# Performance work log

Hardware: AMD Instinct MI355X
Metric: run time of the kernel (lower is better)

Reference implementation:

```python
import jax, jax.numpy as jnp
import numpy as np

N = 8192        # number of nodes
D_FEAT = 64     # feature dim
K = 16          # k_samples
DEG = 32        # max neighbors per node (adj built with <= DEG ones per row)
NEG = -1e30     # mask value for duplicate candidates


def setup_inputs() -> dict:
    key = jax.random.key(0)
    k1, k2, k3 = jax.random.split(key, 3)
    x = jax.random.normal(k1, (N, D_FEAT), dtype=jnp.float32)
    # adjacency with up to DEG random neighbors per row (collisions just lower degree)
    nbr = jax.random.randint(k2, (N, DEG), 0, N)
    adj = jnp.zeros((N, N), jnp.float32).at[jnp.arange(N)[:, None], nbr].set(1.0)
    current_samples = jax.random.randint(k3, (N, K), 0, N).astype(jnp.int32)
    return {"x": x, "adj": adj, "current_samples": current_samples}


def reference(x, adj, current_samples):
    n = x.shape[0]
    # padded neighbor extraction: rows of adj have at most DEG ones, so top_k of the
    # row recovers all neighbor indices; empty slots (value 0) are remapped to the
    # node itself, whose own samples are already in the candidate pool, so the
    # unique candidate set matches the torch adjacency-list construction exactly.
    vals, nbr = jax.lax.top_k(adj, DEG)                       # [N, DEG]
    self_idx = jnp.broadcast_to(jnp.arange(n, dtype=nbr.dtype)[:, None], nbr.shape)
    nbr = jnp.where(vals > 0, nbr, self_idx)
    # candidate pool: neighbor samples flattened + own samples  -> [N, C]
    cand = jnp.concatenate([current_samples[nbr].reshape(n, -1), current_samples], axis=1)
    # emulate torch.unique (sorted, dedup): sort and mask non-first occurrences
    cand = jnp.sort(cand, axis=1)                             # [N, C]
    is_first = jnp.concatenate(
        [jnp.ones((n, 1), bool), cand[:, 1:] != cand[:, :-1]], axis=1)
    # similarities x[i] . x[cand] via one gemm + gather (avoids [N, C, d] gather)
    sim_all = x @ x.T                                         # [N, N]
    sim = jnp.take_along_axis(sim_all, cand, axis=1)          # [N, C]
    sim = jnp.where(is_first, sim, NEG)                       # duplicates masked out
    top_sim, top_idx = jax.lax.top_k(sim, K)                  # [N, K]
    selected = jnp.take_along_axis(cand, top_idx, axis=1)     # [N, K]
    # rare branch: fewer than K unique candidates -> sorted uniques + pad with own samples
    nu = is_first.sum(axis=1, keepdims=True)                  # [N, 1] unique counts
    pos = jnp.cumsum(is_first, axis=1) - 1
    pos = jnp.where(is_first, pos, K)                         # dup / overflow -> dropped
    uniq_k = jnp.zeros((n, K), cand.dtype).at[
        jnp.arange(n)[:, None], pos].set(cand, mode='drop')
    j = jnp.arange(K)[None, :]
    pad = jnp.take_along_axis(current_samples, jnp.clip(j - nu, 0, K - 1), axis=1)
    out = jnp.where(nu >= K, selected, jnp.where(j < nu, uniq_k, pad))
    return out
```

## Files before the change

kernel.cpp:

```cpp
#include <hip/hip_runtime.h>
#include <math.h>

#define NN   8192
#define DF   64
#define KK   16
#define MAXNBR 33
#define NT   256
#define NBINS 2048
#define MAXC 544
#define NR   9
#define HIDX(b) ((((b) & 7) << 8) | ((b) >> 3))

typedef unsigned uvec4 __attribute__((ext_vector_type(4)));

__device__ __forceinline__ unsigned long long kmax(unsigned long long a, unsigned long long b) {
    return a > b ? a : b;
}
__device__ __forceinline__ unsigned long long kmin(unsigned long long a, unsigned long long b) {
    return a > b ? b : a;
}

__device__ __forceinline__ float row_reduce16(float acc) {
    acc += __uint_as_float(__builtin_amdgcn_update_dpp(
        0, (int)__float_as_uint(acc), 0x128, 0xF, 0xF, true));
    acc += __uint_as_float(__builtin_amdgcn_update_dpp(
        0, (int)__float_as_uint(acc), 0x124, 0xF, 0xF, true));
    acc += __uint_as_float(__builtin_amdgcn_update_dpp(
        0, (int)__float_as_uint(acc), 0x122, 0xF, 0xF, true));
    acc += __uint_as_float(__builtin_amdgcn_update_dpp(
        0, (int)__float_as_uint(acc), 0x121, 0xF, 0xF, true));
    return acc;
}

__device__ __forceinline__ void sort64_desc(unsigned long long& kv, int lane) {
    #pragma unroll
    for (int k = 2; k <= 64; k <<= 1) {
        #pragma unroll
        for (int j = k >> 1; j > 0; j >>= 1) {
            unsigned long long o = __shfl_xor(kv, j);
            bool tmax = (((lane & j) == 0) != ((lane & k) != 0));
            kv = tmax ? kmax(kv, o) : kmin(kv, o);
        }
    }
}

__global__ __launch_bounds__(NT, 8)
void fused_kernel(const float* __restrict__ x,
                  const uvec4* __restrict__ adj4,
                  const int*   __restrict__ cs,
                  int*         __restrict__ out)
{
    const int i    = blockIdx.x;
    const int t    = threadIdx.x;
    const int w    = t >> 6;
    const int lane = t & 63;

    __shared__ unsigned mask[NN / 32];
    __shared__ int nbrs[MAXNBR];
    __shared__ int nnbr;
    __shared__ alignas(16) int cand[MAXC];
    __shared__ int ncand;
    __shared__ unsigned long long histsurv[NBINS / 2];
    __shared__ unsigned sum256[NT];
    __shared__ int nsurv;
    __shared__ int B_sh;
    unsigned* const hist = reinterpret_cast<unsigned*>(histsurv);
    unsigned long long* const surv = histsurv;

    if (t < NN / 32) mask[t] = 0u;
    #pragma unroll
    for (int r = 0; r < 4; ++r) histsurv[t + NT * r] = 0ULL;
    cand[t] = 0; cand[t + NT] = 0;
    if (t < MAXC - 2 * NT) cand[t + 2 * NT] = 0;
    if (t == 0) { nbrs[0] = i; nnbr = 1; ncand = 0; nsurv = 0; }
    __syncthreads();

    const uvec4* __restrict__ row4 = adj4 + (size_t)i * (NN / 4);
    uvec4 v[8];
    #pragma unroll
    for (int u = 0; u < 8; ++u) v[u] = __builtin_nontemporal_load(&row4[t + NT * u]);
    #pragma unroll
    for (int u = 0; u < 8; ++u) {
        if ((v[u].x | v[u].y | v[u].z | v[u].w) != 0u) {
            const int base = 4 * (t + NT * u);
            const unsigned e[4] = {v[u].x, v[u].y, v[u].z, v[u].w};
            #pragma unroll
            for (int c2 = 0; c2 < 4; ++c2) {
                if (e[c2] != 0u) {
                    int s = atomicAdd(&nnbr, 1);
                    if (s < MAXNBR) nbrs[s] = base + c2;
                }
            }
        }
    }
    __syncthreads();

    const int M = min(nnbr, MAXNBR);
    const int total = M * KK;

    #pragma unroll
    for (int r = 0; r < 2; ++r) {
        int q = t + NT * r;
        if (q < total) {
            int vv = cs[(size_t)nbrs[q >> 4] * KK + (q & 15)];
            unsigned bit = 1u << (vv & 31);
            unsigned old = atomicOr(&mask[vv >> 5], bit);
            if (!(old & bit)) { int s = atomicAdd(&ncand, 1); cand[s] = vv; }
        }
    }
    const int q2 = 2 * NT + (t - 64);
    if (t >= 64 && t < 80 && q2 < total) {
        int vv = cs[(size_t)nbrs[q2 >> 4] * KK + (q2 & 15)];
        unsigned bit = 1u << (vv & 31);
        unsigned old = atomicOr(&mask[vv >> 5], bit);
        if (!(old & bit)) { int s = atomicAdd(&ncand, 1); cand[s] = vv; }
    }
    __syncthreads();

    const int ncv = ncand;

    const int g  = t >> 4;
    const int gl = t & 15;
    const float4 xi4 = reinterpret_cast<const float4*>(x + (size_t)i * DF)[gl];
    unsigned long long rkeys[NR];
    #pragma unroll
    for (int r = 0; r < NR; ++r) {
        unsigned long long key = 0ULL;
        const int c0 = 4 * g + 64 * r;
        if (c0 < ncv) {
            const int4 c4 = *reinterpret_cast<const int4*>(&cand[c0]);
            const float4 xv0 = reinterpret_cast<const float4*>(x + (size_t)c4.x * DF)[gl];
            const float4 xv1 = reinterpret_cast<const float4*>(x + (size_t)c4.y * DF)[gl];
            const float4 xv2 = reinterpret_cast<const float4*>(x + (size_t)c4.z * DF)[gl];
            const float4 xv3 = reinterpret_cast<const float4*>(x + (size_t)c4.w * DF)[gl];
            float a0 = 0.f, a1 = 0.f, a2 = 0.f, a3 = 0.f;
            a0 = fmaf(xi4.x, xv0.x, a0); a0 = fmaf(xi4.y, xv0.y, a0);
            a0 = fmaf(xi4.z, xv0.z, a0); a0 = fmaf(xi4.w, xv0.w, a0);
            a1 = fmaf(xi4.x, xv1.x, a1); a1 = fmaf(xi4.y, xv1.y, a1);
            a1 = fmaf(xi4.z, xv1.z, a1); a1 = fmaf(xi4.w, xv1.w, a1);
            a2 = fmaf(xi4.x, xv2.x, a2); a2 = fmaf(xi4.y, xv2.y, a2);
            a2 = fmaf(xi4.z, xv2.z, a2); a2 = fmaf(xi4.w, xv2.w, a2);
            a3 = fmaf(xi4.x, xv3.x, a3); a3 = fmaf(xi4.y, xv3.y, a3);
            a3 = fmaf(xi4.z, xv3.z, a3); a3 = fmaf(xi4.w, xv3.w, a3);
            a0 = row_reduce16(a0);
            a1 = row_reduce16(a1);
            a2 = row_reduce16(a2);
            a3 = row_reduce16(a3);
            if (gl < 4 && c0 + gl < ncv) {
                float av = (gl == 0) ? a0 : (gl == 1) ? a1 : (gl == 2) ? a2 : a3;
                int  vb = (gl == 0) ? c4.x : (gl == 1) ? c4.y : (gl == 2) ? c4.z : c4.w;
                unsigned fb = __float_as_uint(av);
                fb = (fb & 0x80000000u) ? ~fb : (fb | 0x80000000u);
                key = ((unsigned long long)fb << 13) |
                      (unsigned long long)(unsigned)(8191 - vb);
                atomicAdd(&hist[HIDX((unsigned)(key >> 34))], 1u);
            }
        }
        rkeys[r] = key;
    }
    __syncthreads();

    if (ncv >= KK) {
        unsigned s8 = 0;
        #pragma unroll
        for (int j = 0; j < 8; ++j) s8 += hist[(j << 8) | t];
        sum256[t] = s8;
        __syncthreads();
        if (w == 0) {
            const int c = 63 - lane;
            unsigned c32 = 0;
            #pragma unroll
            for (int j = 0; j < 4; ++j) c32 += sum256[4 * c + j];
            unsigned p = c32;
            #pragma unroll
            for (int off = 1; off < 64; off <<= 1) {
                unsigned o = __shfl_up(p, off);
                if (lane >= off) p += o;
            }
            unsigned long long bal = __ballot(p >= (unsigned)KK);
            int l1 = (int)__ffsll((unsigned long long)bal) - 1;
            unsigned above1 = __shfl(p - c32, l1);
            int C = 63 - l1;
            int b = 32 * C + 31 - lane;
            unsigned hb = (lane < 32) ? hist[HIDX(b)] : 0u;
            unsigned p2 = hb;
            #pragma unroll
            for (int off = 1; off < 64; off <<= 1) {
                unsigned o = __shfl_up(p2, off);
                if (lane >= off) p2 += o;
            }
            unsigned long long bal2 = __ballot(above1 + p2 >= (unsigned)KK);
            int l2 = (int)__ffsll((unsigned long long)bal2) - 1;
            if (lane == 0) B_sh = 32 * C + 31 - l2;
        }
        __syncthreads();
        const unsigned Bv = (unsigned)B_sh;

        #pragma unroll
        for (int r = 0; r < NR; ++r) {
            unsigned long long k = rkeys[r];
            if (k != 0ULL && (unsigned)(k >> 34) >= Bv) {
                int s = atomicAdd(&nsurv, 1);
                surv[s] = k;
            }
        }
        __syncthreads();

        if (w == 0) {
            const int S = nsurv;
            unsigned long long kk = (lane < S) ? surv[lane] : 0ULL;
            sort64_desc(kk, lane);
            int processed = 64;
            while (processed < S) {
                if (lane >= 16) {
                    int idx = processed + (lane - 16);
                    kk = (idx < S) ? surv[idx] : 0ULL;
                }
                sort64_desc(kk, lane);
                processed += 48;
            }
            if (lane < KK)
                out[(size_t)i * KK + lane] = 8191 - (int)(kk & 0x1FFFULL);
        }
    } else {
        if (t == 0) {
            int sorted_u[KK];
            int cnt2 = 0;
            for (int mw = 0; mw < NN / 32 && cnt2 < KK; ++mw) {
                unsigned b = mask[mw];
                while (b && cnt2 < KK) {
                    int bit = __ffs(b) - 1;
                    b &= b - 1;
                    sorted_u[cnt2++] = mw * 32 + bit;
                }
            }
            for (int j = 0; j < KK; ++j) {
                int uu;
                if (j < ncv) {
                    uu = sorted_u[j];
                } else {
                    int idx = j - ncv;
                    if (idx > KK - 1) idx = KK - 1;
                    uu = cs[(size_t)i * KK + idx];
                }
                out[(size_t)i * KK + j] = uu;
            }
        }
    }
}

extern "C" void kernel_launch(void* const* d_in, const int* in_sizes, int n_in,
                              void* d_out, int out_size, void* d_ws, size_t ws_size,
                              hipStream_t stream)
{
    const float* x   = (const float*)d_in[0];
    const float* adj = (const float*)d_in[1];
    const int*   cs  = (const int*)d_in[2];
    int* out = (int*)d_out;

    fused_kernel<<<NN, NT, 0, stream>>>(
        x, reinterpret_cast<const uvec4*>(adj), cs, out);
}
```

Before: 83.79 us.

## Process four nodes per block and prefetch next adjacency row during selection

Each block now handles four consecutive nodes in a loop, issuing the next node's 32KB adjacency row load right after the similarity phase so it overlaps the histogram/threshold/sort work. Barriers are replaced by a custom s_waitcnt lgkmcnt + s_barrier that avoids waiting on outstanding global loads. This reduces grid size to NN/4 and reuses LDS state with explicit resets, at the cost of fewer blocks in flight and a serial dependency per block.

```diff
diff --git a/kernel.cpp b/kernel.cpp
--- a/kernel.cpp
+++ b/kernel.cpp
@@ -6,12 +6,17 @@
 #define KK   16
 #define MAXNBR 33
 #define NT   256
+#define NPB  4
 #define NBINS 2048
 #define MAXC 544
 #define NR   9
 #define HIDX(b) ((((b) & 7) << 8) | ((b) >> 3))
 
 typedef unsigned uvec4 __attribute__((ext_vector_type(4)));
+
+__device__ __forceinline__ void lds_barrier() {
+    asm volatile("s_waitcnt lgkmcnt(0)\n\ts_barrier" ::: "memory");
+}
 
 __device__ __forceinline__ unsigned long long kmax(unsigned long long a, unsigned long long b) {
     return a > b ? a : b;
@@ -50,201 +55,237 @@
                   const int*   __restrict__ cs,
                   int*         __restrict__ out)
 {
-    const int i    = blockIdx.x;
     const int t    = threadIdx.x;
     const int w    = t >> 6;
     const int lane = t & 63;
+    const int n0   = blockIdx.x * NPB;
 
     __shared__ unsigned mask[NN / 32];
     __shared__ int nbrs[MAXNBR];
-    __shared__ int nnbr;
+    __shared__ int cnts[4];
     __shared__ alignas(16) int cand[MAXC];
-    __shared__ int ncand;
     __shared__ unsigned long long histsurv[NBINS / 2];
     __shared__ unsigned sum256[NT];
-    __shared__ int nsurv;
-    __shared__ int B_sh;
     unsigned* const hist = reinterpret_cast<unsigned*>(histsurv);
     unsigned long long* const surv = histsurv;
 
+    uvec4 v[8];
+
+    {
+        const uvec4* __restrict__ r4 = adj4 + (size_t)n0 * (NN / 4);
+        #pragma unroll
+        for (int u = 0; u < 8; ++u) v[u] = __builtin_nontemporal_load(&r4[t + NT * u]);
+    }
     if (t < NN / 32) mask[t] = 0u;
     #pragma unroll
     for (int r = 0; r < 4; ++r) histsurv[t + NT * r] = 0ULL;
     cand[t] = 0; cand[t + NT] = 0;
     if (t < MAXC - 2 * NT) cand[t + 2 * NT] = 0;
-    if (t == 0) { nbrs[0] = i; nnbr = 1; ncand = 0; nsurv = 0; }
-    __syncthreads();
-
-    const uvec4* __restrict__ row4 = adj4 + (size_t)i * (NN / 4);
-    uvec4 v[8];
-    #pragma unroll
-    for (int u = 0; u < 8; ++u) v[u] = __builtin_nontemporal_load(&row4[t + NT * u]);
+    if (t == 0) { nbrs[0] = n0; cnts[0] = 1; cnts[1] = 0; cnts[2] = 0; }
+    lds_barrier();
+    asm volatile("s_waitcnt vmcnt(0)" ::: "memory");
     #pragma unroll
     for (int u = 0; u < 8; ++u) {
         if ((v[u].x | v[u].y | v[u].z | v[u].w) != 0u) {
             const int base = 4 * (t + NT * u);
             const unsigned e[4] = {v[u].x, v[u].y, v[u].z, v[u].w};
             #pragma unroll
-            for (int c2 = 0; c2 < 4; ++c2) {
+            for (int c2 = 0; c2 < 4; ++c2)
                 if (e[c2] != 0u) {
-                    int s = atomicAdd(&nnbr, 1);
+                    int s = atomicAdd(&cnts[0], 1);
                     if (s < MAXNBR) nbrs[s] = base + c2;
                 }
-            }
         }
     }
-    __syncthreads();
-
-    const int M = min(nnbr, MAXNBR);
-    const int total = M * KK;
-
-    #pragma unroll
-    for (int r = 0; r < 2; ++r) {
-        int q = t + NT * r;
-        if (q < total) {
-            int vv = cs[(size_t)nbrs[q >> 4] * KK + (q & 15)];
+    lds_barrier();
+
+    for (int k = 0; k < NPB; ++k) {
+        const int node = n0 + k;
+        const bool more = (k + 1 < NPB);
+
+        const int M = min(cnts[0], MAXNBR);
+        const int total = M * KK;
+
+        #pragma unroll
+        for (int r = 0; r < 2; ++r) {
+            int q = t + NT * r;
+            if (q < total) {
+                int vv = cs[(size_t)nbrs[q >> 4] * KK + (q & 15)];
+                unsigned bit = 1u << (vv & 31);
+                unsigned old = atomicOr(&mask[vv >> 5], bit);
+                if (!(old & bit)) { int s = atomicAdd(&cnts[1], 1); cand[s] = vv; }
+            }
+        }
+        const int q2 = 2 * NT + (t - 64);
+        if (t >= 64 && t < 80 && q2 < total) {
+            int vv = cs[(size_t)nbrs[q2 >> 4] * KK + (q2 & 15)];
             unsigned bit = 1u << (vv & 31);
             unsigned old = atomicOr(&mask[vv >> 5], bit);
-            if (!(old & bit)) { int s = atomicAdd(&ncand, 1); cand[s] = vv; }
-        }
-    }
-    const int q2 = 2 * NT + (t - 64);
-    if (t >= 64 && t < 80 && q2 < total) {
-        int vv = cs[(size_t)nbrs[q2 >> 4] * KK + (q2 & 15)];
-        unsigned bit = 1u << (vv & 31);
-        unsigned old = atomicOr(&mask[vv >> 5], bit);
-        if (!(old & bit)) { int s = atomicAdd(&ncand, 1); cand[s] = vv; }
-    }
-    __syncthreads();
-
-    const int ncv = ncand;
-
-    const int g  = t >> 4;
-    const int gl = t & 15;
-    const float4 xi4 = reinterpret_cast<const float4*>(x + (size_t)i * DF)[gl];
-    unsigned long long rkeys[NR];
-    #pragma unroll
-    for (int r = 0; r < NR; ++r) {
-        unsigned long long key = 0ULL;
-        const int c0 = 4 * g + 64 * r;
-        if (c0 < ncv) {
-            const int4 c4 = *reinterpret_cast<const int4*>(&cand[c0]);
-            const float4 xv0 = reinterpret_cast<const float4*>(x + (size_t)c4.x * DF)[gl];
-            const float4 xv1 = reinterpret_cast<const float4*>(x + (size_t)c4.y * DF)[gl];
-            const float4 xv2 = reinterpret_cast<const float4*>(x + (size_t)c4.z * DF)[gl];
-            const float4 xv3 = reinterpret_cast<const float4*>(x + (size_t)c4.w * DF)[gl];
-            float a0 = 0.f, a1 = 0.f, a2 = 0.f, a3 = 0.f;
-            a0 = fmaf(xi4.x, xv0.x, a0); a0 = fmaf(xi4.y, xv0.y, a0);
-            a0 = fmaf(xi4.z, xv0.z, a0); a0 = fmaf(xi4.w, xv0.w, a0);
-            a1 = fmaf(xi4.x, xv1.x, a1); a1 = fmaf(xi4.y, xv1.y, a1);
-            a1 = fmaf(xi4.z, xv1.z, a1); a1 = fmaf(xi4.w, xv1.w, a1);
-            a2 = fmaf(xi4.x, xv2.x, a2); a2 = fmaf(xi4.y, xv2.y, a2);
-            a2 = fmaf(xi4.z, xv2.z, a2); a2 = fmaf(xi4.w, xv2.w, a2);
-            a3 = fmaf(xi4.x, xv3.x, a3); a3 = fmaf(xi4.y, xv3.y, a3);
-            a3 = fmaf(xi4.z, xv3.z, a3); a3 = fmaf(xi4.w, xv3.w, a3);
-            a0 = row_reduce16(a0);
-            a1 = row_reduce16(a1);
-            a2 = row_reduce16(a2);
-            a3 = row_reduce16(a3);
-            if (gl < 4 && c0 + gl < ncv) {
-                float av = (gl == 0) ? a0 : (gl == 1) ? a1 : (gl == 2) ? a2 : a3;
-                int  vb = (gl == 0) ? c4.x : (gl == 1) ? c4.y : (gl == 2) ? c4.z : c4.w;
-                unsigned fb = __float_as_uint(av);
-                fb = (fb & 0x80000000u) ? ~fb : (fb | 0x80000000u);
-                key = ((unsigned long long)fb << 13) |
-                      (unsigned long long)(unsigned)(8191 - vb);
-                atomicAdd(&hist[HIDX((unsigned)(key >> 34))], 1u);
-            }
-        }
-        rkeys[r] = key;
-    }
-    __syncthreads();
-
-    if (ncv >= KK) {
-        unsigned s8 = 0;
-        #pragma unroll
-        for (int j = 0; j < 8; ++j) s8 += hist[(j << 8) | t];
-        sum256[t] = s8;
-        __syncthreads();
-        if (w == 0) {
-            const int c = 63 - lane;
-            unsigned c32 = 0;
-            #pragma unroll
-            for (int j = 0; j < 4; ++j) c32 += sum256[4 * c + j];
-            unsigned p = c32;
-            #pragma unroll
-            for (int off = 1; off < 64; off <<= 1) {
-                unsigned o = __shfl_up(p, off);
-                if (lane >= off) p += o;
-            }
-            unsigned long long bal = __ballot(p >= (unsigned)KK);
-            int l1 = (int)__ffsll((unsigned long long)bal) - 1;
-            unsigned above1 = __shfl(p - c32, l1);
-            int C = 63 - l1;
-            int b = 32 * C + 31 - lane;
-            unsigned hb = (lane < 32) ? hist[HIDX(b)] : 0u;
-            unsigned p2 = hb;
-            #pragma unroll
-            for (int off = 1; off < 64; off <<= 1) {
-                unsigned o = __shfl_up(p2, off);
-                if (lane >= off) p2 += o;
-            }
-            unsigned long long bal2 = __ballot(above1 + p2 >= (unsigned)KK);
-            int l2 = (int)__ffsll((unsigned long long)bal2) - 1;
-            if (lane == 0) B_sh = 32 * C + 31 - l2;
-        }
-        __syncthreads();
-        const unsigned Bv = (unsigned)B_sh;
-
+            if (!(old & bit)) { int s = atomicAdd(&cnts[1], 1); cand[s] = vv; }
+        }
+        lds_barrier();
+
+        const int ncv = cnts[1];
+
+        const int g  = t >> 4;
+        const int gl = t & 15;
+        const float4 xi4 = reinterpret_cast<const float4*>(x + (size_t)node * DF)[gl];
+        unsigned long long rkeys[NR];
         #pragma unroll
         for (int r = 0; r < NR; ++r) {
-            unsigned long long k = rkeys[r];
-            if (k != 0ULL && (unsigned)(k >> 34) >= Bv) {
-                int s = atomicAdd(&nsurv, 1);
-                surv[s] = k;
-            }
-        }
-        __syncthreads();
-
-        if (w == 0) {
-            const int S = nsurv;
-            unsigned long long kk = (lane < S) ? surv[lane] : 0ULL;
-            sort64_desc(kk, lane);
-            int processed = 64;
-            while (processed < S) {
-                if (lane >= 16) {
-                    int idx = processed + (lane - 16);
-                    kk = (idx < S) ? surv[idx] : 0ULL;
-                }
+            unsigned long long key = 0ULL;
+            const int c0 = 4 * g + 64 * r;
+            if (c0 < ncv) {
+                const int4 c4 = *reinterpret_cast<const int4*>(&cand[c0]);
+                const float4 xv0 = reinterpret_cast<const float4*>(x + (size_t)c4.x * DF)[gl];
+                const float4 xv1 = reinterpret_cast<const float4*>(x + (size_t)c4.y * DF)[gl];
+                const float4 xv2 = reinterpret_cast<const float4*>(x + (size_t)c4.z * DF)[gl];
+                const float4 xv3 = reinterpret_cast<const float4*>(x + (size_t)c4.w * DF)[gl];
+                float a0 = 0.f, a1 = 0.f, a2 = 0.f, a3 = 0.f;
+                a0 = fmaf(xi4.x, xv0.x, a0); a0 = fmaf(xi4.y, xv0.y, a0);
+                a0 = fmaf(xi4.z, xv0.z, a0); a0 = fmaf(xi4.w, xv0.w, a0);
+                a1 = fmaf(xi4.x, xv1.x, a1); a1 = fmaf(xi4.y, xv1.y, a1);
+                a1 = fmaf(xi4.z, xv1.z, a1); a1 = fmaf(xi4.w, xv1.w, a1);
+                a2 = fmaf(xi4.x, xv2.x, a2); a2 = fmaf(xi4.y, xv2.y, a2);
+                a2 = fmaf(xi4.z, xv2.z, a2); a2 = fmaf(xi4.w, xv2.w, a2);
+                a3 = fmaf(xi4.x, xv3.x, a3); a3 = fmaf(xi4.y, xv3.y, a3);
+                a3 = fmaf(xi4.z, xv3.z, a3); a3 = fmaf(xi4.w, xv3.w, a3);
+                a0 = row_reduce16(a0);
+                a1 = row_reduce16(a1);
+                a2 = row_reduce16(a2);
+                a3 = row_reduce16(a3);
+                if (gl < 4 && c0 + gl < ncv) {
+                    float av = (gl == 0) ? a0 : (gl == 1) ? a1 : (gl == 2) ? a2 : a3;
+                    int  vb = (gl == 0) ? c4.x : (gl == 1) ? c4.y : (gl == 2) ? c4.z : c4.w;
+                    unsigned fb = __float_as_uint(av);
+                    fb = (fb & 0x80000000u) ? ~fb : (fb | 0x80000000u);
+                    key = ((unsigned long long)fb << 13) |
+                          (unsigned long long)(unsigned)(8191 - vb);
+                    atomicAdd(&hist[HIDX((unsigned)(key >> 34))], 1u);
+                }
+            }
+            rkeys[r] = key;
+        }
+        lds_barrier();
+
+        if (more) {
+            const uvec4* __restrict__ r4 = adj4 + (size_t)(node + 1) * (NN / 4);
+            #pragma unroll
+            for (int u = 0; u < 8; ++u) v[u] = __builtin_nontemporal_load(&r4[t + NT * u]);
+        }
+
+        if (ncv >= KK) {
+            unsigned s8 = 0;
+            #pragma unroll
+            for (int j = 0; j < 8; ++j) s8 += hist[(j << 8) | t];
+            sum256[t] = s8;
+            lds_barrier();
+            if (w == 0) {
+                const int c = 63 - lane;
+                unsigned c32 = 0;
+                #pragma unroll
+                for (int j = 0; j < 4; ++j) c32 += sum256[4 * c + j];
+                unsigned p = c32;
+                #pragma unroll
+                for (int off = 1; off < 64; off <<= 1) {
+                    unsigned o = __shfl_up(p, off);
+                    if (lane >= off) p += o;
+                }
+                unsigned long long bal = __ballot(p >= (unsigned)KK);
+                int l1 = (int)__ffsll((unsigned long long)bal) - 1;
+                unsigned above1 = __shfl(p - c32, l1);
+                int C = 63 - l1;
+                int b = 32 * C + 31 - lane;
+                unsigned hb = (lane < 32) ? hist[HIDX(b)] : 0u;
+                unsigned p2 = hb;
+                #pragma unroll
+                for (int off = 1; off < 64; off <<= 1) {
+                    unsigned o = __shfl_up(p2, off);
+                    if (lane >= off) p2 += o;
+                }
+                unsigned long long bal2 = __ballot(above1 + p2 >= (unsigned)KK);
+                int l2 = (int)__ffsll((unsigned long long)bal2) - 1;
+                if (lane == 0) cnts[3] = 32 * C + 31 - l2;
+            }
+            lds_barrier();
+            const unsigned Bv = (unsigned)cnts[3];
+
+            #pragma unroll
+            for (int r = 0; r < NR; ++r) {
+                unsigned long long kq = rkeys[r];
+                if (kq != 0ULL && (unsigned)(kq >> 34) >= Bv) {
+                    int s = atomicAdd(&cnts[2], 1);
+                    surv[s] = kq;
+                }
+            }
+            lds_barrier();
+
+            if (w == 0) {
+                const int S = cnts[2];
+                unsigned long long kk = (lane < S) ? surv[lane] : 0ULL;
                 sort64_desc(kk, lane);
-                processed += 48;
-            }
-            if (lane < KK)
-                out[(size_t)i * KK + lane] = 8191 - (int)(kk & 0x1FFFULL);
-        }
-    } else {
-        if (t == 0) {
-            int sorted_u[KK];
-            int cnt2 = 0;
-            for (int mw = 0; mw < NN / 32 && cnt2 < KK; ++mw) {
-                unsigned b = mask[mw];
-                while (b && cnt2 < KK) {
-                    int bit = __ffs(b) - 1;
-                    b &= b - 1;
-                    sorted_u[cnt2++] = mw * 32 + bit;
-                }
-            }
-            for (int j = 0; j < KK; ++j) {
-                int uu;
-                if (j < ncv) {
-                    uu = sorted_u[j];
-                } else {
-                    int idx = j - ncv;
-                    if (idx > KK - 1) idx = KK - 1;
-                    uu = cs[(size_t)i * KK + idx];
-                }
-                out[(size_t)i * KK + j] = uu;
-            }
+                int processed = 64;
+                while (processed < S) {
+                    if (lane >= 16) {
+                        int idx = processed + (lane - 16);
+                        kk = (idx < S) ? surv[idx] : 0ULL;
+                    }
+                    sort64_desc(kk, lane);
+                    processed += 48;
+                }
+                if (lane < KK)
+                    out[(size_t)node * KK + lane] = 8191 - (int)(kk & 0x1FFFULL);
+            }
+        } else {
+            if (t == 0) {
+                int sorted_u[KK];
+                int cnt2 = 0;
+                for (int mw = 0; mw < NN / 32 && cnt2 < KK; ++mw) {
+                    unsigned b = mask[mw];
+                    while (b && cnt2 < KK) {
+                        int bit = __ffs(b) - 1;
+                        b &= b - 1;
+                        sorted_u[cnt2++] = mw * 32 + bit;
+                    }
+                }
+                for (int j = 0; j < KK; ++j) {
+                    int uu;
+                    if (j < ncv) {
+                        uu = sorted_u[j];
+                    } else {
+                        int idx = j - ncv;
+                        if (idx > KK - 1) idx = KK - 1;
+                        uu = cs[(size_t)node * KK + idx];
+                    }
+                    out[(size_t)node * KK + j] = uu;
+                }
+            }
+        }
+        lds_barrier();
+
+        if (more) {
+            if (t < NN / 32) mask[t] = 0u;
+            #pragma unroll
+            for (int r = 0; r < 4; ++r) histsurv[t + NT * r] = 0ULL;
+            cand[t] = 0; cand[t + NT] = 0;
+            if (t < MAXC - 2 * NT) cand[t + 2 * NT] = 0;
+            if (t == 0) { nbrs[0] = node + 1; cnts[0] = 1; cnts[1] = 0; cnts[2] = 0; }
+            lds_barrier();
+            asm volatile("s_waitcnt vmcnt(0)" ::: "memory");
+            #pragma unroll
+            for (int u = 0; u < 8; ++u) {
+                if ((v[u].x | v[u].y | v[u].z | v[u].w) != 0u) {
+                    const int base = 4 * (t + NT * u);
+                    const unsigned e[4] = {v[u].x, v[u].y, v[u].z, v[u].w};
+                    #pragma unroll
+                    for (int c2 = 0; c2 < 4; ++c2)
+                        if (e[c2] != 0u) {
+                            int s = atomicAdd(&cnts[0], 1);
+                            if (s < MAXNBR) nbrs[s] = base + c2;
+                        }
+                }
+            }
+            lds_barrier();
         }
     }
 }
@@ -258,6 +299,6 @@
     const int*   cs  = (const int*)d_in[2];
     int* out = (int*)d_out;
 
-    fused_kernel<<<NN, NT, 0, stream>>>(
+    fused_kernel<<<NN / NPB, NT, 0, stream>>>(
         x, reinterpret_cast<const uvec4*>(adj), cs, out);
 }
```

Result: slower. 194.6 us (+132.2%).
